# Optimization experiments

Hardware: AMD Instinct MI355X
Metric: run time of the kernel (lower is better)

## Reference

```python
import jax, jax.numpy as jnp
import numpy as np

N_NODES = 50000


def _gcn(x, row, col, w, b, n):
    # add self loops
    loops = jnp.arange(n, dtype=row.dtype)
    row = jnp.concatenate([row, loops])
    col = jnp.concatenate([col, loops])
    h = x @ w  # [N, out]
    deg = jax.ops.segment_sum(jnp.ones(col.shape, h.dtype), col, num_segments=n)
    dinv = jnp.where(deg > 0, deg ** -0.5, 0.0)
    norm = dinv[row] * dinv[col]  # [E+N]
    msg = norm[:, None] * h[row]
    out = jax.ops.segment_sum(msg, col, num_segments=n)
    return out + b


def _edgeconv(x, row, col, w1, b1, w2, b2, n):
    x_i = x[col]            # target features
    x_j = x[row]            # source features
    t = jnp.concatenate([x_i, x_j - x_i], axis=1)  # [E, 2*hidden]
    m = jax.nn.relu(t @ w1 + b1) @ w2 + b2          # [E, hidden]
    agg = jax.ops.segment_max(m, col, num_segments=n)
    # PyG fills empty segments with 0, segment_max fills with -inf
    return jnp.where(jnp.isfinite(agg), agg, 0.0)


def setup_inputs() -> dict:
    key = jax.random.key(0)
    ks = jax.random.split(key, 10)
    n, e = N_NODES, 800000
    cin, ch, cout = 32, 64, 16
    x = jax.random.normal(ks[0], (n, cin), dtype=jnp.float32)
    edge_index = jax.random.randint(ks[1], (2, e), 0, n, dtype=jnp.int64)

    def glorot(k, shape):
        lim = (6.0 / (shape[0] + shape[1])) ** 0.5
        return jax.random.uniform(k, shape, jnp.float32, -lim, lim)

    return {
        "x": x,
        "edge_index": edge_index,
        "gcn1_w": glorot(ks[2], (cin, ch)),
        "gcn1_b": jnp.zeros((ch,), jnp.float32),
        "edge_w1": glorot(ks[3], (2 * ch, ch)),
        "edge_b1": jnp.zeros((ch,), jnp.float32),
        "edge_w2": glorot(ks[4], (ch, ch)),
        "edge_b2": jnp.zeros((ch,), jnp.float32),
        "gcn2_w": glorot(ks[5], (ch, cout)),
        "gcn2_b": jnp.zeros((cout,), jnp.float32),
    }


def reference(x, edge_index, gcn1_w, gcn1_b, edge_w1, edge_b1, edge_w2, edge_b2, gcn2_w, gcn2_b):
    n = x.shape[0]
    row, col = edge_index[0], edge_index[1]
    h = jnp.tanh(_gcn(x, row, col, gcn1_w, gcn1_b, n))
    h = jax.nn.relu(_edgeconv(h, row, col, edge_w1, edge_b1, edge_w2, edge_b2, n))
    out = _gcn(h, row, col, gcn2_w, gcn2_b, n)
    return out
```

## Files before the change

### kernel.cpp

```cpp
#include <hip/hip_runtime.h>


typedef __attribute__((ext_vector_type(8))) short short8;
typedef __attribute__((ext_vector_type(4))) float f32x4;
typedef __attribute__((ext_vector_type(8))) _Float16 f16x8;
typedef __attribute__((ext_vector_type(4))) _Float16 f16x4;
typedef __attribute__((ext_vector_type(2))) _Float16 f16x2;

#define FILL_CH 4096

__device__ __forceinline__ unsigned short f2bf(float x) {
    unsigned int u = __float_as_uint(x);
    return (unsigned short)((u + 0x7FFFu + ((u >> 16) & 1u)) >> 16);
}
__device__ __forceinline__ float bf2f(unsigned short h) {
    return __uint_as_float(((unsigned int)h) << 16);
}
__device__ __forceinline__ void splitT(float u, short& hi, short& lo) {
    unsigned int ub = __float_as_uint(u);
    hi = (short)(ub >> 16);
    float r = u - __uint_as_float(ub & 0xFFFF0000u);
    lo = (short)(__float_as_uint(r) >> 16);
}
__device__ __forceinline__ f16x8 relu8(f16x8 v) {
    f16x8 z = {0, 0, 0, 0, 0, 0, 0, 0};
#if __has_builtin(__builtin_elementwise_max)
    return __builtin_elementwise_max(v, z);
#else
    f16x8 o;
#pragma unroll
    for (int j = 0; j < 8; ++j) o[j] = v[j] > (_Float16)0 ? v[j] : (_Float16)0;
    return o;
#endif
}

#define ROR_ADD(s, CTRL)                                                         \
    s += __int_as_float(__builtin_amdgcn_update_dpp(                             \
        0, __float_as_int(s), (CTRL), 0xf, 0xf, false))
#define ROR8_ADD(s) ROR_ADD(s, 0x128)

__global__ __launch_bounds__(256) void k_fill_a(
        const int* __restrict__ row, const int* __restrict__ col,
        int* __restrict__ bcnt, int* __restrict__ stage, int E, int nb) {
    __shared__ int cnt[512];
    __shared__ int base[512];
    int tid = threadIdx.x;
    for (int i = tid; i < nb; i += 256) cnt[i] = 0;
    __syncthreads();
    int e0 = blockIdx.x * FILL_CH;
    int r[16], c[16];
#pragma unroll
    for (int i = 0; i < 16; ++i) {
        int e = e0 + tid + i * 256;
        if (e < E) {
            r[i] = row[e]; c[i] = col[e];
            atomicAdd(&cnt[c[i] >> 7], 1);
        } else c[i] = -1;
    }
    __syncthreads();
    for (int i = tid; i < nb; i += 256)
        base[i] = cnt[i] ? (i << 12) + atomicAdd(&bcnt[i], cnt[i]) : 0;
    __syncthreads();
#pragma unroll
    for (int i = 0; i < 16; ++i) {
        if (c[i] >= 0) {
            int b = c[i] >> 7;
            int lp = atomicAdd(&base[b], 1);
            stage[lp] = (r[i] << 7) | (c[i] & 127);
        }
    }
}

__global__ __launch_bounds__(256) void k_fill_b2(
        const int* __restrict__ bcnt, const int* __restrict__ stage,
        const float4* __restrict__ x4, f16x4* __restrict__ xh4,
        int* __restrict__ ptr, float* __restrict__ dinv, int* __restrict__ csr,
        int n, int nb, int E) {
    __shared__ int lcnt[128];
    __shared__ int lcur[128];
    __shared__ float dinvS[128];
    __shared__ int wtotS;
    __shared__ int wsum[4];
    __shared__ int gbaseS;
    int b = blockIdx.x, tid = threadIdx.x;
    int lane = tid & 63, w = tid >> 6;
    int c0 = b << 7;
    int s0 = b << 12;
    int tot = bcnt[b];
    if (tid < 128) lcnt[tid] = 0;
    int acc = 0;
    if (tid < b && tid < nb) acc += bcnt[tid];
    int t2 = tid + 256;
    if (t2 < b && t2 < nb) acc += bcnt[t2];
#pragma unroll
    for (int off = 1; off < 64; off <<= 1) acc += __shfl_xor(acc, off);
    if (lane == 0) wsum[w] = acc;
    __syncthreads();
    if (tid == 0) {
        gbaseS = wsum[0] + wsum[1] + wsum[2] + wsum[3];
        if (b == nb - 1) ptr[n] = E;
    }
    for (int p = tid; p < tot; p += 256)
        atomicAdd(&lcnt[stage[s0 + p] & 127], 1);
    __syncthreads();
    int gbase = gbaseS;
    int v = (tid < 128) ? lcnt[tid] : 0;
    int s = v;
    for (int off = 1; off < 64; off <<= 1) {
        int t = __shfl_up(s, off, 64);
        if (lane >= off) s += t;
    }
    if (tid == 63) wtotS = s;
    __syncthreads();
    int excl = s - v + ((w == 1) ? wtotS : 0);
    if (tid < 128) {
        int c = c0 + tid;
        int basep = gbase + excl;
        lcur[tid] = basep;
        float dv = rsqrtf((float)(v + 1));
        dinvS[tid] = dv;
        if (c < n) {
            ptr[c] = basep;
            dinv[c] = dv;
        }
    }
    __syncthreads();
    for (int p = tid; p < tot; p += 256) {
        int vv = stage[s0 + p];
        int pos = atomicAdd(&lcur[vv & 127], 1);
        csr[pos] = vv >> 7;
    }
    int cmax = n - c0; if (cmax > 128) cmax = 128;
    for (int i = tid; i < cmax * 8; i += 256) {
        int ci = i >> 3, j = i & 7;
        float dv = dinvS[ci];
        float4 xv = x4[(size_t)(c0 + ci) * 8 + j];
        f16x4 o;
        o[0] = (_Float16)(dv * xv.x); o[1] = (_Float16)(dv * xv.y);
        o[2] = (_Float16)(dv * xv.z); o[3] = (_Float16)(dv * xv.w);
        xh4[(size_t)(c0 + ci) * 8 + j] = o;
    }
}

__global__ __launch_bounds__(256) void k_gather32(
        const int* __restrict__ ptr, const int* __restrict__ csr_row,
        const float* __restrict__ x, const _Float16* __restrict__ xh,
        const float* __restrict__ dinv, float* __restrict__ agg, int n) {
    int lane = threadIdx.x & 63;
    int f4 = lane & 7, slot = lane >> 3;
    const f16x4* xh4 = (const f16x4*)xh;

    int nwaves = gridDim.x * 4;
    int wid = blockIdx.x * 4 + (threadIdx.x >> 6);
    if (wid >= n) return;

    int c = wid;
    int st = ptr[c], ed = ptr[c + 1];
    int r0 = (st + slot < ed) ? csr_row[st + slot] : 0;
    while (true) {
        int cn = c + nwaves;
        bool hasN = cn < n;
        int stn = 0, edn = 0;
        if (hasN) { stn = ptr[cn]; edn = ptr[cn + 1]; }

        float sx = 0.f, sy = 0.f, sz = 0.f, sw = 0.f;
        int p = st + slot;
        int r = r0;
        while (p < ed) {
            int rcur = r;
            int pn = p + 8;
            if (pn < ed) r = csr_row[pn];
            f16x4 xv = xh4[(size_t)rcur * 8 + f4];
            sx += (float)xv[0];
            sy += (float)xv[1];
            sz += (float)xv[2];
            sw += (float)xv[3];
            p = pn;
        }
        int r0n = 0;
        if (hasN && stn + slot < edn) r0n = csr_row[stn + slot];

        ROR8_ADD(sx); ROR8_ADD(sy); ROR8_ADD(sz); ROR8_ADD(sw);
#pragma unroll
        for (int off = 16; off < 64; off <<= 1) {
            sx += __shfl_xor(sx, off); sy += __shfl_xor(sy, off);
            sz += __shfl_xor(sz, off); sw += __shfl_xor(sw, off);
        }
        if (slot == 0) {
            float dv = dinv[c], d2 = dv * dv;
            float4 xv = ((const float4*)x)[(size_t)c * 8 + f4];
            float4 o;
            o.x = dv * sx + d2 * xv.x;
            o.y = dv * sy + d2 * xv.y;
            o.z = dv * sz + d2 * xv.z;
            o.w = dv * sw + d2 * xv.w;
            ((float4*)agg)[(size_t)c * 8 + f4] = o;
        }
        if (!hasN) break;
        c = cn; st = stn; ed = edn; r0 = r0n;
    }
}

__global__ __launch_bounds__(256, 1) void k_h1tab(
        const float* __restrict__ agg, const float* __restrict__ gw,
        const float* __restrict__ gb, const float* __restrict__ w1,
        const float* __restrict__ b1,
        _Float16* __restrict__ atab, _Float16* __restrict__ btab, int ntiles) {
    __shared__ float tileS[4][16 * 66];
    int lane = threadIdx.x & 63;
    int wv = threadIdx.x >> 6;
    int n16 = lane & 15, q = lane >> 4;
    float* T = tileS[wv];

    short8 gh[4], gl[4];
    float gbias[4];
#pragma unroll
    for (int t = 0; t < 4; ++t) {
        gbias[t] = gb[t * 16 + n16];
        short8 hh, ll;
#pragma unroll
        for (int j = 0; j < 8; ++j) {
            float w = gw[(q * 8 + j) * 64 + t * 16 + n16];
            unsigned short wh = f2bf(w);
            hh[j] = (short)wh;
            ll[j] = (short)f2bf(w - bf2f(wh));
        }
        gh[t] = hh; gl[t] = ll;
    }
    short8 th[4][2], tl[4][2], uh[4][2], ul[4][2];
    float bias1[4];
#pragma unroll
    for (int t = 0; t < 4; ++t) {
        bias1[t] = b1[t * 16 + n16];
#pragma unroll
        for (int ck = 0; ck < 2; ++ck) {
            short8 h1v, l1v, h2v, l2v;
#pragma unroll
            for (int j = 0; j < 8; ++j) {
                int d = ck * 32 + q * 8 + j;
                float wbv = w1[(64 + d) * 64 + t * 16 + n16];
                float wtv = w1[d * 64 + t * 16 + n16] - wbv;
                unsigned short x1 = f2bf(wtv);
                h1v[j] = (short)x1; l1v[j] = (short)f2bf(wtv - bf2f(x1));
                unsigned short x2 = f2bf(wbv);
                h2v[j] = (short)x2; l2v[j] = (short)f2bf(wbv - bf2f(x2));
            }
            th[t][ck] = h1v; tl[t][ck] = l1v;
            uh[t][ck] = h2v; ul[t][ck] = l2v;
        }
    }

    int nwaves = gridDim.x * 4;
    int wid = blockIdx.x * 4 + wv;
    for (int tile = wid; tile < ntiles; tile += nwaves) {
        int v0 = tile * 16;
        const float4* a4 = (const float4*)(agg + (size_t)(v0 + n16) * 32);
        float4 A0 = a4[2 * q], A1 = a4[2 * q + 1];
        float a[8] = {A0.x, A0.y, A0.z, A0.w, A1.x, A1.y, A1.z, A1.w};
        short8 ah, al;
#pragma unroll
        for (int j = 0; j < 8; ++j) { short h, l; splitT(a[j], h, l); ah[j] = h; al[j] = l; }
#pragma unroll
        for (int t = 0; t < 4; ++t) {
            f32x4 acc = (f32x4){gbias[t], gbias[t], gbias[t], gbias[t]};
            acc = __builtin_amdgcn_mfma_f32_16x16x32_bf16(ah, gh[t], acc, 0, 0, 0);
            acc = __builtin_amdgcn_mfma_f32_16x16x32_bf16(al, gh[t], acc, 0, 0, 0);
            acc = __builtin_amdgcn_mfma_f32_16x16x32_bf16(ah, gl[t], acc, 0, 0, 0);
#pragma unroll
            for (int i = 0; i < 4; ++i)
                T[(q * 4 + i) * 66 + t * 16 + n16] = tanhf(acc[i]);
        }
        float b[16];
#pragma unroll
        for (int j = 0; j < 8; ++j) {
            b[j]     = T[n16 * 66 + q * 8 + j];
            b[8 + j] = T[n16 * 66 + 32 + q * 8 + j];
        }
        short8 ah0, ah1, al0, al1;
#pragma unroll
        for (int j = 0; j < 8; ++j) {
            short h, l;
            splitT(b[j], h, l);      ah0[j] = h; al0[j] = l;
            splitT(b[8 + j], h, l);  ah1[j] = h; al1[j] = l;
        }
#pragma unroll
        for (int t = 0; t < 4; ++t) {
            f32x4 aa = (f32x4){bias1[t], bias1[t], bias1[t], bias1[t]};
            aa = __builtin_amdgcn_mfma_f32_16x16x32_bf16(ah0, th[t][0], aa, 0, 0, 0);
            aa = __builtin_amdgcn_mfma_f32_16x16x32_bf16(ah1, th[t][1], aa, 0, 0, 0);
            aa = __builtin_amdgcn_mfma_f32_16x16x32_bf16(al0, th[t][0], aa, 0, 0, 0);
            aa = __builtin_amdgcn_mfma_f32_16x16x32_bf16(al1, th[t][1], aa, 0, 0, 0);
            aa = __builtin_amdgcn_mfma_f32_16x16x32_bf16(ah0, tl[t][0], aa, 0, 0, 0);
            aa = __builtin_amdgcn_mfma_f32_16x16x32_bf16(ah1, tl[t][1], aa, 0, 0, 0);
            f32x4 bb = (f32x4){0.f, 0.f, 0.f, 0.f};
            bb = __builtin_amdgcn_mfma_f32_16x16x32_bf16(ah0, uh[t][0], bb, 0, 0, 0);
            bb = __builtin_amdgcn_mfma_f32_16x16x32_bf16(ah1, uh[t][1], bb, 0, 0, 0);
            bb = __builtin_amdgcn_mfma_f32_16x16x32_bf16(al0, uh[t][0], bb, 0, 0, 0);
            bb = __builtin_amdgcn_mfma_f32_16x16x32_bf16(al1, uh[t][1], bb, 0, 0, 0);
            bb = __builtin_amdgcn_mfma_f32_16x16x32_bf16(ah0, ul[t][0], bb, 0, 0, 0);
            bb = __builtin_amdgcn_mfma_f32_16x16x32_bf16(ah1, ul[t][1], bb, 0, 0, 0);
#pragma unroll
            for (int i = 0; i < 4; ++i) {
                size_t off = (size_t)(v0 + q * 4 + i) * 64 + t * 16 + n16;
                atab[off] = (_Float16)aa[i];
                btab[off] = (_Float16)bb[i];
            }
        }
    }
}

__global__ __launch_bounds__(256) void k_edge_mlp(
        const int* __restrict__ ptr, const int* __restrict__ csr_row,
        const _Float16* __restrict__ atab, const _Float16* __restrict__ btab,
        const float* __restrict__ w2, const float* __restrict__ b2,
        const float* __restrict__ wg, const float* __restrict__ dinv,
        _Float16* __restrict__ h2h, int n) {
    int lane = threadIdx.x & 63;
    int n16 = lane & 15, q = lane >> 4;

    f16x8 wh[4][2];
    float bias[4];
    float wgf[4][4];
#pragma unroll
    for (int t = 0; t < 4; ++t) {
        bias[t] = b2[t * 16 + n16];
#pragma unroll
        for (int jj = 0; jj < 4; ++jj)
            wgf[t][jj] = wg[(t * 16 + n16) * 16 + q * 4 + jj];
#pragma unroll
        for (int ck = 0; ck < 2; ++ck) {
            f16x8 hh;
#pragma unroll
            for (int j = 0; j < 8; ++j)
                hh[j] = (_Float16)w2[(ck * 32 + q * 8 + j) * 64 + t * 16 + n16];
            wh[t][ck] = hh;
        }
    }
    const f32x4 z4 = (f32x4){0.f, 0.f, 0.f, 0.f};

    int nwaves = gridDim.x * 4;
    int wid = blockIdx.x * 4 + (threadIdx.x >> 6);
    if (wid >= n) return;

    int c = wid;
    int st = ptr[c], ed = ptr[c + 1];
    float dv = dinv[c];
    {
        int deg = ed - st;
        int nf = deg >> 4, rm = deg & 15;
        int rrem0 = (rm > 0 && n16 < rm) ? csr_row[st + (nf << 4) + n16] : 0;
        int r0 = (nf > 0) ? csr_row[st + n16] : 0;
        int r = r0, rrem = rrem0;
        while (true) {
            int cn = c + nwaves;
            bool hasN = cn < n;
            int stn = 0, edn = 0;
            float dvn = 0.f;
            if (hasN) { stn = ptr[cn]; edn = ptr[cn + 1]; dvn = dinv[cn]; }

            const f16x8* a8 = (const f16x8*)(atab + (size_t)c * 64);
            f16x8 A0 = a8[q], A1 = a8[4 + q];
            float red[4] = {0.f, 0.f, 0.f, 0.f};

            int deg2 = ed - st;
            int nfull = deg2 >> 4;
            int rem = deg2 & 15;
            for (int ft = 0; ft < nfull; ++ft) {
                int rcur = r;
                if (ft + 1 < nfull) r = csr_row[st + (ft + 1) * 16 + n16];
                const f16x8* b8 = (const f16x8*)(btab + (size_t)rcur * 64);
                f16x8 u0 = relu8(A0 + b8[q]);
                f16x8 u1 = relu8(A1 + b8[4 + q]);
                __builtin_amdgcn_s_setprio(1);
#pragma unroll
                for (int t = 0; t < 4; ++t) {
                    f32x4 a = __builtin_amdgcn_mfma_f32_16x16x32_f16(u0, wh[t][0], z4, 0, 0, 0);
                    a = __builtin_amdgcn_mfma_f32_16x16x32_f16(u1, wh[t][1], a, 0, 0, 0);
                    float mx = fmaxf(fmaxf(a[0], a[1]), fmaxf(a[2], a[3]));
                    red[t] = fmaxf(red[t], mx + bias[t]);
                }
                __builtin_amdgcn_s_setprio(0);
            }
            if (rem > 0) {
                f16x8 u0 = {0, 0, 0, 0, 0, 0, 0, 0};
                f16x8 u1 = {0, 0, 0, 0, 0, 0, 0, 0};
                if (n16 < rem) {
                    const f16x8* b8 = (const f16x8*)(btab + (size_t)rrem * 64);
                    u0 = relu8(A0 + b8[q]);
                    u1 = relu8(A1 + b8[4 + q]);
                }
                __builtin_amdgcn_s_setprio(1);
#pragma unroll
                for (int t = 0; t < 4; ++t) {
                    f32x4 a = __builtin_amdgcn_mfma_f32_16x16x32_f16(u0, wh[t][0], z4, 0, 0, 0);
                    a = __builtin_amdgcn_mfma_f32_16x16x32_f16(u1, wh[t][1], a, 0, 0, 0);
#pragma unroll
                    for (int i = 0; i < 4; ++i)
                        if (q * 4 + i < rem) red[t] = fmaxf(red[t], a[i] + bias[t]);
                }
                __builtin_amdgcn_s_setprio(0);
            }

            int rn = 0, rremn = 0;
            if (hasN) {
                int degn = edn - stn;
                int nfn = degn >> 4, rmn = degn & 15;
                if (rmn > 0 && n16 < rmn) rremn = csr_row[stn + (nfn << 4) + n16];
                if (nfn > 0) rn = csr_row[stn + n16];
            }

#pragma unroll
            for (int t = 0; t < 4; ++t) {
                red[t] = fmaxf(red[t], __shfl_xor(red[t], 16));
                red[t] = fmaxf(red[t], __shfl_xor(red[t], 32));
            }
            float part[4];
#pragma unroll
            for (int jj = 0; jj < 4; ++jj) {
                part[jj] = red[0] * wgf[0][jj];
                part[jj] = fmaf(red[1], wgf[1][jj], part[jj]);
                part[jj] = fmaf(red[2], wgf[2][jj], part[jj]);
                part[jj] = fmaf(red[3], wgf[3][jj], part[jj]);
                ROR_ADD(part[jj], 0x121);
                ROR_ADD(part[jj], 0x122);
                ROR_ADD(part[jj], 0x124);
                ROR_ADD(part[jj], 0x128);
            }
            if (n16 == 0) {
                f16x4 ph;
                ph[0] = (_Float16)(dv * part[0]); ph[1] = (_Float16)(dv * part[1]);
                ph[2] = (_Float16)(dv * part[2]); ph[3] = (_Float16)(dv * part[3]);
                ((f16x4*)(h2h + (size_t)c * 16))[q] = ph;
            }

            if (!hasN) break;
            c = cn; st = stn; ed = edn; r = rn; rrem = rremn; dv = dvn;
        }
    }
}

__global__ __launch_bounds__(256) void k_gcn2_gather(
        const int* __restrict__ ptr, const int* __restrict__ csr_row,
        const _Float16* __restrict__ h2h, const float* __restrict__ dinv,
        const float* __restrict__ bg, float* __restrict__ out, int n) {
    int lane = threadIdx.x & 63;
    int f2 = lane & 7, slot = lane >> 3;
    const f16x2* h22 = (const f16x2*)h2h;

    int nwaves = gridDim.x * 4;
    int wid = blockIdx.x * 4 + (threadIdx.x >> 6);
    if (wid >= n) return;

    int c = wid;
    int st = ptr[c], ed = ptr[c + 1];
    int r0 = (st + slot < ed) ? csr_row[st + slot] : 0;
    while (true) {
        int cn = c + nwaves;
        bool hasN = cn < n;
        int stn = 0, edn = 0;
        if (hasN) { stn = ptr[cn]; edn = ptr[cn + 1]; }

        float sx = 0.f, sy = 0.f;
        int p = st + slot;
        int r = r0;
        while (p < ed) {
            int rcur = r;
            int pn = p + 8;
            if (pn < ed) r = csr_row[pn];
            f16x2 hv = h22[(size_t)rcur * 8 + f2];
            sx += (float)hv[0];
            sy += (float)hv[1];
            p = pn;
        }
        int r0n = 0;
        if (hasN && stn + slot < edn) r0n = csr_row[stn + slot];

        ROR8_ADD(sx); ROR8_ADD(sy);
#pragma unroll
        for (int off = 16; off < 64; off <<= 1) {
            sx += __shfl_xor(sx, off);
            sy += __shfl_xor(sy, off);
        }
        if (slot == 0) {
            float dv = dinv[c];
            f16x2 hv = h22[(size_t)c * 8 + f2];
            float2 o;
            o.x = bg[2 * f2]     + dv * ((float)hv[0] + sx);
            o.y = bg[2 * f2 + 1] + dv * ((float)hv[1] + sy);
            ((float2*)out)[(size_t)c * 8 + f2] = o;
        }
        if (!hasN) break;
        c = cn; st = stn; ed = edn; r0 = r0n;
    }
}

extern "C" void kernel_launch(void* const* d_in, const int* in_sizes, int n_in,
                              void* d_out, int out_size, void* d_ws, size_t ws_size,
                              hipStream_t stream) {
    const float* x   = (const float*)d_in[0];
    const int*   ei  = (const int*)d_in[1];
    const float* g1w = (const float*)d_in[2];
    const float* g1b = (const float*)d_in[3];
    const float* ew1 = (const float*)d_in[4];
    const float* eb1 = (const float*)d_in[5];
    const float* ew2 = (const float*)d_in[6];
    const float* eb2 = (const float*)d_in[7];
    const float* g2w = (const float*)d_in[8];
    const float* g2b = (const float*)d_in[9];
    float* out = (float*)d_out;
    float* ws  = (float*)d_ws;

    const int n = in_sizes[0] / 32;
    const int E = in_sizes[1] / 2;
    const int* row = ei;
    const int* col = ei + E;
    const int ntiles = (n + 15) / 16;
    const int nbuck = (n + 127) >> 7;

    size_t npad    = ((size_t)n + 63) & ~(size_t)63;
    size_t o_misc  = 0;
    size_t o_ptr   = 1024;
    size_t o_csr   = o_ptr + npad + 64;
    size_t o_dinv  = o_csr + (size_t)E;
    size_t o_atab  = o_dinv + npad;
    size_t o_btab  = o_atab + (size_t)n * 32;
    size_t o_agg   = o_btab + (size_t)n * 32;
    size_t o_xh    = o_agg + (size_t)n * 32;
    size_t o_h2h   = o_xh + (size_t)n * 16;
    size_t o_stage = o_h2h + (size_t)n * 8;

    int*      bcnt   = (int*)(ws + o_misc);
    int*      ptr    = (int*)(ws + o_ptr);
    int*      csr    = (int*)(ws + o_csr);
    float*    dinv   = ws + o_dinv;
    _Float16* atab   = (_Float16*)(ws + o_atab);
    _Float16* btab   = (_Float16*)(ws + o_btab);
    float*    agg    = ws + o_agg;
    _Float16* xh     = (_Float16*)(ws + o_xh);
    _Float16* h2h    = (_Float16*)(ws + o_h2h);
    int*      stage  = (int*)(ws + o_stage);

    int fill_nb = (E + FILL_CH - 1) / FILL_CH;

    hipMemsetAsync(bcnt, 0, 512 * sizeof(int), stream);
    k_fill_a<<<fill_nb, 256, 0, stream>>>(row, col, bcnt, stage, E, nbuck);
    k_fill_b2<<<nbuck, 256, 0, stream>>>(bcnt, stage, (const float4*)x, (f16x4*)xh,
                                         ptr, dinv, csr, n, nbuck, E);
    k_gather32<<<2048, 256, 0, stream>>>(ptr, csr, x, xh, dinv, agg, n);
    k_h1tab<<<256, 256, 0, stream>>>(agg, g1w, g1b, ew1, eb1, atab, btab, ntiles);
    k_edge_mlp<<<2048, 256, 0, stream>>>(ptr, csr, atab, btab, ew2, eb2, g2w,
                                         dinv, h2h, n);
    k_gcn2_gather<<<2048, 256, 0, stream>>>(ptr, csr, h2h, dinv, g2b, out, n);
}
```

Before: 179.6 us.

## Fuse memset and two CSR build kernels into one cooperative kernel

Replaces the memset plus the two-kernel bucket fill (count/stage, then per-bucket CSR build) with a single cooperative kernel that uses grid-wide syncs between the zeroing, staging and CSR phases. This removes two launch boundaries and the memset dispatch. The grid is nbuck blocks (about 391), which must all be co-resident, and fillNb (about 196) must not exceed it. Grid syncs carry their own cost and may lower occupancy.

```diff
diff --git a/kernel.cpp b/kernel.cpp
--- a/kernel.cpp
+++ b/kernel.cpp
@@ -1,4 +1,7 @@
 #include <hip/hip_runtime.h>
+#include <hip/hip_cooperative_groups.h>
+
+namespace cg = cooperative_groups;
 
 
 typedef __attribute__((ext_vector_type(8))) short short8;
@@ -39,51 +42,57 @@
         0, __float_as_int(s), (CTRL), 0xf, 0xf, false))
 #define ROR8_ADD(s) ROR_ADD(s, 0x128)
 
-__global__ __launch_bounds__(256) void k_fill_a(
+__global__ __launch_bounds__(256) void k_build(
         const int* __restrict__ row, const int* __restrict__ col,
-        int* __restrict__ bcnt, int* __restrict__ stage, int E, int nb) {
+        const float4* __restrict__ x4, f16x4* __restrict__ xh4,
+        int* __restrict__ bcnt, int* __restrict__ stage,
+        int* __restrict__ ptr, float* __restrict__ dinv, int* __restrict__ csr,
+        int E, int n, int nb, int fillNb) {
+    cg::grid_group grid = cg::this_grid();
     __shared__ int cnt[512];
     __shared__ int base[512];
-    int tid = threadIdx.x;
-    for (int i = tid; i < nb; i += 256) cnt[i] = 0;
-    __syncthreads();
-    int e0 = blockIdx.x * FILL_CH;
-    int r[16], c[16];
-#pragma unroll
-    for (int i = 0; i < 16; ++i) {
-        int e = e0 + tid + i * 256;
-        if (e < E) {
-            r[i] = row[e]; c[i] = col[e];
-            atomicAdd(&cnt[c[i] >> 7], 1);
-        } else c[i] = -1;
-    }
-    __syncthreads();
-    for (int i = tid; i < nb; i += 256)
-        base[i] = cnt[i] ? (i << 12) + atomicAdd(&bcnt[i], cnt[i]) : 0;
-    __syncthreads();
-#pragma unroll
-    for (int i = 0; i < 16; ++i) {
-        if (c[i] >= 0) {
-            int b = c[i] >> 7;
-            int lp = atomicAdd(&base[b], 1);
-            stage[lp] = (r[i] << 7) | (c[i] & 127);
-        }
-    }
-}
-
-__global__ __launch_bounds__(256) void k_fill_b2(
-        const int* __restrict__ bcnt, const int* __restrict__ stage,
-        const float4* __restrict__ x4, f16x4* __restrict__ xh4,
-        int* __restrict__ ptr, float* __restrict__ dinv, int* __restrict__ csr,
-        int n, int nb, int E) {
     __shared__ int lcnt[128];
     __shared__ int lcur[128];
     __shared__ float dinvS[128];
     __shared__ int wtotS;
     __shared__ int wsum[4];
     __shared__ int gbaseS;
+
     int b = blockIdx.x, tid = threadIdx.x;
     int lane = tid & 63, w = tid >> 6;
+
+    if (b == 0)
+        for (int i = tid; i < 512; i += 256) bcnt[i] = 0;
+    grid.sync();
+
+    if (b < fillNb) {
+        for (int i = tid; i < nb; i += 256) cnt[i] = 0;
+        __syncthreads();
+        int e0 = b * FILL_CH;
+        int r[16], c[16];
+#pragma unroll
+        for (int i = 0; i < 16; ++i) {
+            int e = e0 + tid + i * 256;
+            if (e < E) {
+                r[i] = row[e]; c[i] = col[e];
+                atomicAdd(&cnt[c[i] >> 7], 1);
+            } else c[i] = -1;
+        }
+        __syncthreads();
+        for (int i = tid; i < nb; i += 256)
+            base[i] = cnt[i] ? (i << 12) + atomicAdd(&bcnt[i], cnt[i]) : 0;
+        __syncthreads();
+#pragma unroll
+        for (int i = 0; i < 16; ++i) {
+            if (c[i] >= 0) {
+                int bb = c[i] >> 7;
+                int lp = atomicAdd(&base[bb], 1);
+                stage[lp] = (r[i] << 7) | (c[i] & 127);
+            }
+        }
+    }
+    grid.sync();
+
     int c0 = b << 7;
     int s0 = b << 12;
     int tot = bcnt[b];
@@ -542,10 +551,18 @@
 
     int fill_nb = (E + FILL_CH - 1) / FILL_CH;
 
-    hipMemsetAsync(bcnt, 0, 512 * sizeof(int), stream);
-    k_fill_a<<<fill_nb, 256, 0, stream>>>(row, col, bcnt, stage, E, nbuck);
-    k_fill_b2<<<nbuck, 256, 0, stream>>>(bcnt, stage, (const float4*)x, (f16x4*)xh,
-                                         ptr, dinv, csr, n, nbuck, E);
+    {
+        const float4* x4p = (const float4*)x;
+        f16x4* xh4p = (f16x4*)xh;
+        int En = E, nn = n, nb = nbuck, fnb = fill_nb;
+        void* args[] = {
+            (void*)&row, (void*)&col, (void*)&x4p, (void*)&xh4p,
+            (void*)&bcnt, (void*)&stage, (void*)&ptr, (void*)&dinv,
+            (void*)&csr, (void*)&En, (void*)&nn, (void*)&nb, (void*)&fnb
+        };
+        hipLaunchCooperativeKernel((const void*)k_build, dim3(nbuck), dim3(256),
+                                   args, 0, stream);
+    }
     k_gather32<<<2048, 256, 0, stream>>>(ptr, csr, x, xh, dinv, agg, n);
     k_h1tab<<<256, 256, 0, stream>>>(agg, g1w, g1b, ew1, eb1, atab, btab, ntiles);
     k_edge_mlp<<<2048, 256, 0, stream>>>(ptr, csr, atab, btab, ew2, eb2, g2w,
```

Result: slower. 276.0 us (+53.7%).
